# Performance work log

Measured on AMD Instinct MI355X. Metric: run time of the kernel, lower is better.

The kernel has to match this reference:

```python
import jax, jax.numpy as jnp
import numpy as np

H, BOTTLENECK, TOPK = 2048, 64, 128
TAU, EPS = 1.0, 1e-20

def setup_inputs() -> dict:
    key = jax.random.key(0)
    ks = jax.random.split(key, 7)
    B, T = 4, 4096
    x = jax.random.normal(ks[0], (B, T, H), dtype=jnp.float32)
    Wd = jax.random.normal(ks[1], (H, BOTTLENECK), dtype=jnp.float32) / np.sqrt(H)
    bd = jax.random.normal(ks[2], (BOTTLENECK,), dtype=jnp.float32) * 0.01
    Wu = jax.random.normal(ks[3], (BOTTLENECK, H), dtype=jnp.float32) / np.sqrt(BOTTLENECK)
    bu = jax.random.normal(ks[4], (H,), dtype=jnp.float32) * 0.01
    Wg = jax.random.normal(ks[5], (H,), dtype=jnp.float32) / np.sqrt(H)
    bg = jax.random.normal(ks[6], (), dtype=jnp.float32) * 0.01
    return {"x": x, "Wd": Wd, "bd": bd, "Wu": Wu, "bu": bu, "Wg": Wg, "bg": bg}

def reference(x, Wd, bd, Wu, bu, Wg, bg):
    B, T, _ = x.shape
    k = max(1, min(T, TOPK))
    # gate logits: Linear(H,1).squeeze(-1) -> [B, T]
    logits = jnp.einsum('bth,h->bt', x, Wg) + bg
    # gumbel noise (fixed key for determinism; non-differentiated like torch)
    U = jax.random.uniform(jax.random.key(42), logits.shape, dtype=logits.dtype)
    g = -jnp.log(-jnp.log(U + EPS) + EPS)
    probs = jax.nn.softmax((logits + g) / TAU, axis=-1)            # [B, T]
    topk_idx = jax.lax.top_k(logits, k)[1]                          # [B, k]
    hard = jnp.zeros_like(logits).at[jnp.arange(B)[:, None], topk_idx].set(1.0)
    mask = jax.lax.stop_gradient(hard - probs) + probs              # straight-through
    # bottleneck adapter
    delta = jnp.maximum(x @ Wd + bd, 0.0) @ Wu + bu                 # [B, T, H]
    return x + delta * mask[..., None]
```

## Files before the change

### kernel.cpp

```cpp
#include <hip/hip_runtime.h>
#include <hip/hip_bf16.h>

#define H 2048
#define BN 64
#define TT 4096
#define BB 4
#define KK 128
#define CP_BLOCKS 1024
#define RPB 4

__global__ __launch_bounds__(256) void copy_logits_kernel(
    const float* __restrict__ x, const float* __restrict__ Wg,
    float* __restrict__ out, float* __restrict__ logits, int nrows) {
    const int lane   = threadIdx.x & 63;
    const int wave   = (blockIdx.x * 256 + threadIdx.x) >> 6;
    const int nwaves = CP_BLOCKS * 4;
    const float4* w4 = (const float4*)Wg;
    float4 w[8];
#pragma unroll
    for (int i = 0; i < 8; ++i) w[i] = w4[lane + 64 * i];

    for (int row = wave; row < nrows; row += nwaves) {
        const float4* x4 = (const float4*)(x + (size_t)row * H);
        float4*       o4 = (float4*)(out + (size_t)row * H);
        float4 a[8];
#pragma unroll
        for (int i = 0; i < 8; ++i) a[i] = x4[lane + 64 * i];
        float s0 = 0.f, s1 = 0.f, s2 = 0.f, s3 = 0.f;
#pragma unroll
        for (int i = 0; i < 8; ++i) {
            o4[lane + 64 * i] = a[i];
            s0 = fmaf(a[i].x, w[i].x, s0);
            s1 = fmaf(a[i].y, w[i].y, s1);
            s2 = fmaf(a[i].z, w[i].z, s2);
            s3 = fmaf(a[i].w, w[i].w, s3);
        }
        float acc = (s0 + s1) + (s2 + s3);
#pragma unroll
        for (int off = 32; off > 0; off >>= 1) acc += __shfl_down(acc, off);
        if (lane == 0) logits[row] = acc;
    }
}

__global__ __launch_bounds__(256) void topk_idx_kernel(
    const float* __restrict__ logits, int* __restrict__ idxlist) {
    __shared__ unsigned keys[TT];
    __shared__ int wsum[4];
    __shared__ int gtp[256], eqp[256];
    const int tid = threadIdx.x;
    const int b   = blockIdx.x;
    const float* lr = logits + (size_t)b * TT;

    for (int i = tid; i < TT; i += 256) {
        unsigned u = __float_as_uint(lr[i]);
        keys[i] = (u & 0x80000000u) ? ~u : (u | 0x80000000u);
    }
    __syncthreads();

    unsigned prefix = 0;
    int k = KK;
    for (int bit = 31; bit >= 0; --bit) {
        unsigned ref = (prefix >> bit) | 1u;
        int c = 0;
        for (int i = tid; i < TT; i += 256) c += ((keys[i] >> bit) == ref);
#pragma unroll
        for (int off = 32; off > 0; off >>= 1) c += __shfl_down(c, off);
        if ((tid & 63) == 0) wsum[tid >> 6] = c;
        __syncthreads();
        int total = wsum[0] + wsum[1] + wsum[2] + wsum[3];
        __syncthreads();
        if (total >= k) prefix |= (1u << bit);
        else            k -= total;
    }

    const int per = TT / 256, i0 = tid * per, i1 = i0 + per;
    int cgt = 0, ceq = 0;
    for (int i = i0; i < i1; ++i) {
        cgt += (keys[i] > prefix);
        ceq += (keys[i] == prefix);
    }
    gtp[tid] = cgt; eqp[tid] = ceq;
    __syncthreads();
    if (tid == 0) {
        int sg = 0, se = 0;
        for (int t = 0; t < 256; ++t) {
            int a = gtp[t]; gtp[t] = sg; sg += a;
            int c = eqp[t]; eqp[t] = se; se += c;
        }
        wsum[0] = sg;
    }
    __syncthreads();
    const int total_gt = wsum[0];
    const int need_eq  = KK - total_gt;
    int g = gtp[tid], e = eqp[tid];
    int* dst = idxlist + b * KK;
    for (int i = i0; i < i1; ++i) {
        if (keys[i] > prefix)       dst[g++] = b * TT + i;
        else if (keys[i] == prefix) { if (e < need_eq) dst[total_gt + e] = b * TT + i; e++; }
    }
}

__global__ __launch_bounds__(512) void adapter_kernel(
    const float* __restrict__ x, const float* __restrict__ Wd,
    const float* __restrict__ bd, const float* __restrict__ Wu,
    const float* __restrict__ bu, const int* __restrict__ idxlist,
    float* __restrict__ out) {
    __shared__ float hp[8][RPB][BN];
    __shared__ float hs[RPB][BN];
    const int tid  = threadIdx.x;
    const int lane = tid & 63;
    const int g    = tid >> 6;

    int rows[RPB];
#pragma unroll
    for (int r = 0; r < RPB; ++r) rows[r] = idxlist[blockIdx.x * RPB + r];

    float xr0[4], xr1[4], xr2[4], xr3[4];
    {
        const float* p0 = x + (size_t)rows[0] * H + g * 256 + lane;
        const float* p1 = x + (size_t)rows[1] * H + g * 256 + lane;
        const float* p2 = x + (size_t)rows[2] * H + g * 256 + lane;
        const float* p3 = x + (size_t)rows[3] * H + g * 256 + lane;
#pragma unroll
        for (int k = 0; k < 4; ++k) {
            xr0[k] = p0[k * 64]; xr1[k] = p1[k * 64];
            xr2[k] = p2[k * 64]; xr3[k] = p3[k * 64];
        }
    }

    float a0 = 0.f, a1 = 0.f, a2 = 0.f, a3 = 0.f;
    const float* wdp = Wd + (size_t)(g * 256) * BN + lane;
#pragma unroll
    for (int k = 0; k < 4; ++k) {
#pragma unroll 8
        for (int l = 0; l < 64; ++l) {
            float wv = wdp[(size_t)(k * 64 + l) * BN];
            a0 = fmaf(__int_as_float(__builtin_amdgcn_readlane(__float_as_int(xr0[k]), l)), wv, a0);
            a1 = fmaf(__int_as_float(__builtin_amdgcn_readlane(__float_as_int(xr1[k]), l)), wv, a1);
            a2 = fmaf(__int_as_float(__builtin_amdgcn_readlane(__float_as_int(xr2[k]), l)), wv, a2);
            a3 = fmaf(__int_as_float(__builtin_amdgcn_readlane(__float_as_int(xr3[k]), l)), wv, a3);
        }
    }
    hp[g][0][lane] = a0; hp[g][1][lane] = a1;
    hp[g][2][lane] = a2; hp[g][3][lane] = a3;
    __syncthreads();

    if (tid < RPB * BN) {
        int r = tid >> 6, jj = tid & 63;
        float v = bd[jj];
#pragma unroll
        for (int gg = 0; gg < 8; ++gg) v += hp[gg][r][jj];
        hs[r][jj] = v > 0.f ? v : 0.f;
    }
    __syncthreads();

    const float4* Wu4 = (const float4*)Wu;
    float4 y0 = ((const float4*)bu)[tid];
    float4 y1 = y0, y2 = y0, y3 = y0;
    for (int jj = 0; jj < BN; ++jj) {
        float4 wv = Wu4[(size_t)jj * (H / 4) + tid];
        float h0 = hs[0][jj], h1 = hs[1][jj], h2 = hs[2][jj], h3 = hs[3][jj];
        y0.x = fmaf(h0, wv.x, y0.x); y0.y = fmaf(h0, wv.y, y0.y);
        y0.z = fmaf(h0, wv.z, y0.z); y0.w = fmaf(h0, wv.w, y0.w);
        y1.x = fmaf(h1, wv.x, y1.x); y1.y = fmaf(h1, wv.y, y1.y);
        y1.z = fmaf(h1, wv.z, y1.z); y1.w = fmaf(h1, wv.w, y1.w);
        y2.x = fmaf(h2, wv.x, y2.x); y2.y = fmaf(h2, wv.y, y2.y);
        y2.z = fmaf(h2, wv.z, y2.z); y2.w = fmaf(h2, wv.w, y2.w);
        y3.x = fmaf(h3, wv.x, y3.x); y3.y = fmaf(h3, wv.y, y3.y);
        y3.z = fmaf(h3, wv.z, y3.z); y3.w = fmaf(h3, wv.w, y3.w);
    }

#pragma unroll
    for (int r = 0; r < RPB; ++r) {
        const float4* xr4 = (const float4*)(x + (size_t)rows[r] * H);
        float4*       o4  = (float4*)(out + (size_t)rows[r] * H);
        float4 xa = xr4[tid];
        float4 yv = (r == 0) ? y0 : (r == 1) ? y1 : (r == 2) ? y2 : y3;
        o4[tid] = make_float4(xa.x + yv.x, xa.y + yv.y, xa.z + yv.z, xa.w + yv.w);
    }
}

extern "C" void kernel_launch(void* const* d_in, const int* in_sizes, int n_in,
                              void* d_out, int out_size, void* d_ws, size_t ws_size,
                              hipStream_t stream) {
    const float* x  = (const float*)d_in[0];
    const float* Wd = (const float*)d_in[1];
    const float* bd = (const float*)d_in[2];
    const float* Wu = (const float*)d_in[3];
    const float* bu = (const float*)d_in[4];
    const float* Wg = (const float*)d_in[5];
    float* out = (float*)d_out;

    const int nrows = in_sizes[0] / H;
    float* logits  = (float*)d_ws;
    int*   idxlist = (int*)((char*)d_ws + (size_t)nrows * sizeof(float));

    copy_logits_kernel<<<CP_BLOCKS, 256, 0, stream>>>(x, Wg, out, logits, nrows);
    topk_idx_kernel<<<BB, 256, 0, stream>>>(logits, idxlist);
    adapter_kernel<<<(BB * KK) / RPB, 512, 0, stream>>>(x, Wd, bd, Wu, bu, idxlist, out);
}
```

Measured before the change: 102.2 us.

## Split logit rows into half-row waves, nontemporal copy stores, 8 rows per adapter block

The copy/logit kernel now gives each wave half a row (1024 floats), writes two partial dot products per row, and uses nontemporal stores for the output copy. It also doubles the grid and adds an occupancy hint. The top-k kernel sums the two partials when it builds the keys. The adapter kernel processes 8 selected rows per block instead of 4, so each Wd/Wu weight load is reused across more rows and half as many blocks are launched. The costs are higher register pressure in the adapter kernel and fewer adapter blocks in flight.

```diff
diff --git a/kernel.cpp b/kernel.cpp
--- a/kernel.cpp
+++ b/kernel.cpp
@@ -6,30 +6,32 @@
 #define TT 4096
 #define BB 4
 #define KK 128
-#define CP_BLOCKS 1024
-#define RPB 4
-
-__global__ __launch_bounds__(256) void copy_logits_kernel(
+#define CP_BLOCKS 2048
+#define RPB 8
+
+typedef float vf4 __attribute__((ext_vector_type(4)));
+
+__global__ __launch_bounds__(256, 8) void copy_logits_kernel(
     const float* __restrict__ x, const float* __restrict__ Wg,
-    float* __restrict__ out, float* __restrict__ logits, int nrows) {
-    const int lane   = threadIdx.x & 63;
-    const int wave   = (blockIdx.x * 256 + threadIdx.x) >> 6;
-    const int nwaves = CP_BLOCKS * 4;
-    const float4* w4 = (const float4*)Wg;
-    float4 w[8];
-#pragma unroll
-    for (int i = 0; i < 8; ++i) w[i] = w4[lane + 64 * i];
-
-    for (int row = wave; row < nrows; row += nwaves) {
-        const float4* x4 = (const float4*)(x + (size_t)row * H);
-        float4*       o4 = (float4*)(out + (size_t)row * H);
-        float4 a[8];
-#pragma unroll
-        for (int i = 0; i < 8; ++i) a[i] = x4[lane + 64 * i];
+    float* __restrict__ out, float* __restrict__ lpart, int nhalf) {
+    const int lane = threadIdx.x & 63;
+    const int wv   = (blockIdx.x * 256 + threadIdx.x) >> 6;
+    const int nw   = CP_BLOCKS * 4;
+    const vf4* w4 = (const vf4*)Wg + (size_t)(wv & 1) * 256;
+    vf4 w[4];
+#pragma unroll
+    for (int i = 0; i < 4; ++i) w[i] = w4[lane + 64 * i];
+
+    for (int hr = wv; hr < nhalf; hr += nw) {
+        const vf4* xs = (const vf4*)x + (size_t)hr * 256;
+        vf4*       os = (vf4*)out + (size_t)hr * 256;
+        vf4 a[4];
+#pragma unroll
+        for (int i = 0; i < 4; ++i) a[i] = xs[lane + 64 * i];
         float s0 = 0.f, s1 = 0.f, s2 = 0.f, s3 = 0.f;
 #pragma unroll
-        for (int i = 0; i < 8; ++i) {
-            o4[lane + 64 * i] = a[i];
+        for (int i = 0; i < 4; ++i) {
+            __builtin_nontemporal_store(a[i], &os[lane + 64 * i]);
             s0 = fmaf(a[i].x, w[i].x, s0);
             s1 = fmaf(a[i].y, w[i].y, s1);
             s2 = fmaf(a[i].z, w[i].z, s2);
@@ -38,21 +40,22 @@
         float acc = (s0 + s1) + (s2 + s3);
 #pragma unroll
         for (int off = 32; off > 0; off >>= 1) acc += __shfl_down(acc, off);
-        if (lane == 0) logits[row] = acc;
+        if (lane == 0) lpart[hr] = acc;
     }
 }
 
 __global__ __launch_bounds__(256) void topk_idx_kernel(
-    const float* __restrict__ logits, int* __restrict__ idxlist) {
+    const float* __restrict__ lpart, int* __restrict__ idxlist) {
     __shared__ unsigned keys[TT];
     __shared__ int wsum[4];
     __shared__ int gtp[256], eqp[256];
     const int tid = threadIdx.x;
     const int b   = blockIdx.x;
-    const float* lr = logits + (size_t)b * TT;
+    const float* lp = lpart + (size_t)b * TT * 2;
 
     for (int i = tid; i < TT; i += 256) {
-        unsigned u = __float_as_uint(lr[i]);
+        float v = lp[2 * i] + lp[2 * i + 1];
+        unsigned u = __float_as_uint(v);
         keys[i] = (u & 0x80000000u) ? ~u : (u | 0x80000000u);
     }
     __syncthreads();
@@ -115,37 +118,34 @@
 #pragma unroll
     for (int r = 0; r < RPB; ++r) rows[r] = idxlist[blockIdx.x * RPB + r];
 
-    float xr0[4], xr1[4], xr2[4], xr3[4];
-    {
-        const float* p0 = x + (size_t)rows[0] * H + g * 256 + lane;
-        const float* p1 = x + (size_t)rows[1] * H + g * 256 + lane;
-        const float* p2 = x + (size_t)rows[2] * H + g * 256 + lane;
-        const float* p3 = x + (size_t)rows[3] * H + g * 256 + lane;
-#pragma unroll
-        for (int k = 0; k < 4; ++k) {
-            xr0[k] = p0[k * 64]; xr1[k] = p1[k * 64];
-            xr2[k] = p2[k * 64]; xr3[k] = p3[k * 64];
-        }
-    }
-
-    float a0 = 0.f, a1 = 0.f, a2 = 0.f, a3 = 0.f;
+    float xr[RPB][4];
+#pragma unroll
+    for (int r = 0; r < RPB; ++r) {
+        const float* p = x + (size_t)rows[r] * H + g * 256 + lane;
+#pragma unroll
+        for (int k = 0; k < 4; ++k) xr[r][k] = p[k * 64];
+    }
+
+    float acc[RPB];
+#pragma unroll
+    for (int r = 0; r < RPB; ++r) acc[r] = 0.f;
     const float* wdp = Wd + (size_t)(g * 256) * BN + lane;
 #pragma unroll
     for (int k = 0; k < 4; ++k) {
 #pragma unroll 8
         for (int l = 0; l < 64; ++l) {
             float wv = wdp[(size_t)(k * 64 + l) * BN];
-            a0 = fmaf(__int_as_float(__builtin_amdgcn_readlane(__float_as_int(xr0[k]), l)), wv, a0);
-            a1 = fmaf(__int_as_float(__builtin_amdgcn_readlane(__float_as_int(xr1[k]), l)), wv, a1);
-            a2 = fmaf(__int_as_float(__builtin_amdgcn_readlane(__float_as_int(xr2[k]), l)), wv, a2);
-            a3 = fmaf(__int_as_float(__builtin_amdgcn_readlane(__float_as_int(xr3[k]), l)), wv, a3);
-        }
-    }
-    hp[g][0][lane] = a0; hp[g][1][lane] = a1;
-    hp[g][2][lane] = a2; hp[g][3][lane] = a3;
-    __syncthreads();
-
-    if (tid < RPB * BN) {
+#pragma unroll
+            for (int r = 0; r < RPB; ++r)
+                acc[r] = fmaf(__int_as_float(__builtin_amdgcn_readlane(
+                                  __float_as_int(xr[r][k]), l)), wv, acc[r]);
+        }
+    }
+#pragma unroll
+    for (int r = 0; r < RPB; ++r) hp[g][r][lane] = acc[r];
+    __syncthreads();
+
+    {
         int r = tid >> 6, jj = tid & 63;
         float v = bd[jj];
 #pragma unroll
@@ -155,28 +155,26 @@
     __syncthreads();
 
     const float4* Wu4 = (const float4*)Wu;
-    float4 y0 = ((const float4*)bu)[tid];
-    float4 y1 = y0, y2 = y0, y3 = y0;
+    float4 yb = ((const float4*)bu)[tid];
+    float4 y[RPB];
+#pragma unroll
+    for (int r = 0; r < RPB; ++r) y[r] = yb;
     for (int jj = 0; jj < BN; ++jj) {
         float4 wv = Wu4[(size_t)jj * (H / 4) + tid];
-        float h0 = hs[0][jj], h1 = hs[1][jj], h2 = hs[2][jj], h3 = hs[3][jj];
-        y0.x = fmaf(h0, wv.x, y0.x); y0.y = fmaf(h0, wv.y, y0.y);
-        y0.z = fmaf(h0, wv.z, y0.z); y0.w = fmaf(h0, wv.w, y0.w);
-        y1.x = fmaf(h1, wv.x, y1.x); y1.y = fmaf(h1, wv.y, y1.y);
-        y1.z = fmaf(h1, wv.z, y1.z); y1.w = fmaf(h1, wv.w, y1.w);
-        y2.x = fmaf(h2, wv.x, y2.x); y2.y = fmaf(h2, wv.y, y2.y);
-        y2.z = fmaf(h2, wv.z, y2.z); y2.w = fmaf(h2, wv.w, y2.w);
-        y3.x = fmaf(h3, wv.x, y3.x); y3.y = fmaf(h3, wv.y, y3.y);
-        y3.z = fmaf(h3, wv.z, y3.z); y3.w = fmaf(h3, wv.w, y3.w);
-    }
-
+#pragma unroll
+        for (int r = 0; r < RPB; ++r) {
+            float h = hs[r][jj];
+            y[r].x = fmaf(h, wv.x, y[r].x); y[r].y = fmaf(h, wv.y, y[r].y);
+            y[r].z = fmaf(h, wv.z, y[r].z); y[r].w = fmaf(h, wv.w, y[r].w);
+        }
+    }
 #pragma unroll
     for (int r = 0; r < RPB; ++r) {
         const float4* xr4 = (const float4*)(x + (size_t)rows[r] * H);
         float4*       o4  = (float4*)(out + (size_t)rows[r] * H);
         float4 xa = xr4[tid];
-        float4 yv = (r == 0) ? y0 : (r == 1) ? y1 : (r == 2) ? y2 : y3;
-        o4[tid] = make_float4(xa.x + yv.x, xa.y + yv.y, xa.z + yv.z, xa.w + yv.w);
+        o4[tid] = make_float4(xa.x + y[r].x, xa.y + y[r].y,
+                              xa.z + y[r].z, xa.w + y[r].w);
     }
 }
 
@@ -192,10 +190,11 @@
     float* out = (float*)d_out;
 
     const int nrows = in_sizes[0] / H;
-    float* logits  = (float*)d_ws;
-    int*   idxlist = (int*)((char*)d_ws + (size_t)nrows * sizeof(float));
-
-    copy_logits_kernel<<<CP_BLOCKS, 256, 0, stream>>>(x, Wg, out, logits, nrows);
-    topk_idx_kernel<<<BB, 256, 0, stream>>>(logits, idxlist);
+    const int nhalf = nrows * 2;
+    float* lpart   = (float*)d_ws;
+    int*   idxlist = (int*)((char*)d_ws + (size_t)nhalf * sizeof(float));
+
+    copy_logits_kernel<<<CP_BLOCKS, 256, 0, stream>>>(x, Wg, out, lpart, nhalf);
+    topk_idx_kernel<<<BB, 256, 0, stream>>>(lpart, idxlist);
     adapter_kernel<<<(BB * KK) / RPB, 512, 0, stream>>>(x, Wd, bd, Wu, bu, idxlist, out);
 }
```

Result: slower. 114.9 us (+12.4%).
